# Kernel optimization log

Measured on AMD Instinct MI355X. Metric: run time of the kernel, lower is better.

The kernel has to match this reference:

```python
import jax, jax.numpy as jnp
import numpy as np

B, N, D = 4, 2048, 512
H = 8
DH = D // H
FF = 2 * D


def setup_inputs() -> dict:
    key = jax.random.key(0)
    ks = jax.random.split(key, 16)
    s = lambda fan_in: 1.0 / np.sqrt(fan_in)
    inp = {
        "x0": jax.random.normal(ks[0], (B, N, D), jnp.float32),
        "x1": jax.random.normal(ks[1], (B, N, D), jnp.float32),
        # projections (torch Linear: weight [out, in])
        "Wqk": jax.random.uniform(ks[2], (D, D), jnp.float32, -s(D), s(D)),
        "bqk": jax.random.uniform(ks[3], (D,), jnp.float32, -s(D), s(D)),
        "Wv": jax.random.uniform(ks[4], (D, D), jnp.float32, -s(D), s(D)),
        "bv": jax.random.uniform(ks[5], (D,), jnp.float32, -s(D), s(D)),
        "Wo": jax.random.uniform(ks[6], (D, D), jnp.float32, -s(D), s(D)),
        "bo": jax.random.uniform(ks[7], (D,), jnp.float32, -s(D), s(D)),
        # FFN: Linear(2D,2D) -> LayerNorm(2D) -> GELU -> Linear(2D,D)
        "Wf1": jax.random.uniform(ks[8], (FF, FF), jnp.float32, -s(FF), s(FF)),
        "bf1": jax.random.uniform(ks[9], (FF,), jnp.float32, -s(FF), s(FF)),
        "ln_g": jnp.ones((FF,), jnp.float32),
        "ln_b": jnp.zeros((FF,), jnp.float32),
        "Wf2": jax.random.uniform(ks[10], (D, FF), jnp.float32, -s(FF), s(FF)),
        "bf2": jax.random.uniform(ks[11], (D,), jnp.float32, -s(FF), s(FF)),
    }
    return inp


def _split_heads(t):
    # [B,N,D] -> [B,H,N,DH]
    return t.reshape(B, N, H, DH).transpose(0, 2, 1, 3)


def _attn(q, k, v):
    # q,k,v: [B,H,N,DH]; scale by sqrt(d_k) as in the torch Attention module
    scores = jnp.einsum("bhnd,bhmd->bhnm", q, k) / jnp.sqrt(jnp.float32(DH))
    attn = jax.nn.softmax(scores, axis=-1)
    return jnp.einsum("bhnm,bhmd->bhnd", attn, v)


def _merge_heads(t):
    # [B,H,N,DH] -> [B,N,D]
    return t.transpose(0, 2, 1, 3).reshape(B, N, D)


def _ffn(x, Wf1, bf1, ln_g, ln_b, Wf2, bf2):
    h = x @ Wf1.T + bf1
    mu = jnp.mean(h, axis=-1, keepdims=True)
    var = jnp.mean(jnp.square(h - mu), axis=-1, keepdims=True)
    h = (h - mu) / jnp.sqrt(var + 1e-5) * ln_g + ln_b
    h = jax.nn.gelu(h, approximate=False)
    return h @ Wf2.T + bf2


def reference(x0, x1, Wqk, bqk, Wv, bv, Wo, bo, Wf1, bf1, ln_g, ln_b, Wf2, bf2):
    qk0 = _split_heads(x0 @ Wqk.T + bqk)
    qk1 = _split_heads(x1 @ Wqk.T + bqk)
    v0 = _split_heads(x0 @ Wv.T + bv)
    v1 = _split_heads(x1 @ Wv.T + bv)

    m0 = _merge_heads(_attn(qk0, qk1, v1)) @ Wo.T + bo
    m1 = _merge_heads(_attn(qk1, qk0, v0)) @ Wo.T + bo

    y0 = x0 + _ffn(jnp.concatenate([x0, m0], -1), Wf1, bf1, ln_g, ln_b, Wf2, bf2)
    y1 = x1 + _ffn(jnp.concatenate([x1, m1], -1), Wf1, bf1, ln_g, ln_b, Wf2, bf2)
    return (y0, y1)
```

## Files before the change

kernel.cpp:

```cpp
#include <hip/hip_runtime.h>
#include <hip/hip_bf16.h>
#include <math.h>

typedef __bf16 bf16;
typedef __bf16 bf16x8 __attribute__((ext_vector_type(8)));
typedef __bf16 bf16x4 __attribute__((ext_vector_type(4)));
typedef float  f32x4  __attribute__((ext_vector_type(4)));

#define DEVI __device__ __forceinline__

DEVI void async16(bf16* lds, const bf16* g) {
    __builtin_amdgcn_global_load_lds(
        (const __attribute__((address_space(1))) unsigned int*)g,
        (__attribute__((address_space(3))) unsigned int*)lds, 16, 0, 0);
}
DEVI f32x4 mfma16(bf16x8 a, bf16x8 b, f32x4 c) {
    return __builtin_amdgcn_mfma_f32_16x16x32_bf16(a, b, c, 0, 0, 0);
}

__global__ __launch_bounds__(256) void prep(
    const float* __restrict__ x0, const float* __restrict__ x1, bf16* __restrict__ Xbf,
    const float* __restrict__ Wqk, const float* __restrict__ Wv,
    const float* __restrict__ Wf1, const float* __restrict__ Wf2,
    bf16* __restrict__ Wqkv, bf16* __restrict__ Wbig, bf16* __restrict__ Wf1Rb,
    bf16* __restrict__ Wf2b,
    const float* __restrict__ Wo, bf16* __restrict__ WoT,
    const float* __restrict__ bo, const float* __restrict__ bf1,
    float* __restrict__ bf1p)
{
    __shared__ float Ls[64][65];
    const int bid = blockIdx.x, t = threadIdx.x;
    if (bid < 8192) {
        long i = (long)bid * 256 + t;
        long r = i >> 7, c = (i & 127) * 4;
        const float* src = (r < 8192) ? (x0 + r * 512 + c) : (x1 + (r - 8192) * 512 + c);
        float4 v = *(const float4*)src;
        bf16x4 o;
        o[0] = (bf16)v.x; o[1] = (bf16)v.y; o[2] = (bf16)v.z; o[3] = (bf16)v.w;
        *(bf16x4*)(Xbf + r * 1024 + c) = o;
    } else if (bid < 10240) {
        long i = (long)(bid - 8192) * 256 + t;
        const float* s; bf16* d;
        if (i < 131072) {
            s = (i < 65536) ? Wqk + i * 4 : Wv + (i - 65536) * 4;
            d = Wqkv + i * 4;
        } else if (i < 393216) {
            long e = (i - 131072) * 4, r = e >> 10, c = e & 1023;
            s = Wf1 + e;
            d = (c < 512) ? (Wbig + r * 1024 + c) : (Wf1Rb + r * 512 + (c - 512));
        } else {
            s = Wf2 + (i - 393216) * 4;
            d = Wf2b + (i - 393216) * 4;
        }
        float4 v = *(const float4*)s;
        bf16x4 o;
        o[0] = (bf16)v.x; o[1] = (bf16)v.y; o[2] = (bf16)v.z; o[3] = (bf16)v.w;
        *(bf16x4*)d = o;
    } else if (bid < 10304) {
        const int bb = bid - 10240;
        const int bi = bb & 7, bj = bb >> 3;
        const int i0 = bi * 64, j0 = bj * 64;
        const int r0 = t >> 4, c4 = (t & 15) * 4;
#pragma unroll
        for (int it = 0; it < 4; it++) {
            int row = r0 + 16 * it;
            float4 v = *(const float4*)(Wo + (long)(i0 + row) * 512 + j0 + c4);
            Ls[row][c4] = v.x; Ls[row][c4 + 1] = v.y;
            Ls[row][c4 + 2] = v.z; Ls[row][c4 + 3] = v.w;
        }
        __syncthreads();
#pragma unroll
        for (int it = 0; it < 4; it++) {
            int orow = r0 + 16 * it;
            bf16x4 o;
#pragma unroll
            for (int k = 0; k < 4; k++) o[k] = (bf16)Ls[c4 + k][orow];
            *(bf16x4*)(WoT + (long)(j0 + orow) * 512 + i0 + c4) = o;
        }
    } else {
        const int w = t >> 6, lane = t & 63;
        const int row = (bid - 10304) * 4 + w;
        const float* rp = Wf1 + (long)row * 1024 + 512 + lane * 8;
        float4 a = *(const float4*)rp;
        float4 b = *(const float4*)(rp + 4);
        const float* bp = bo + lane * 8;
        float4 c = *(const float4*)bp;
        float4 d = *(const float4*)(bp + 4);
        float s = a.x * c.x + a.y * c.y + a.z * c.z + a.w * c.w +
                  b.x * d.x + b.y * d.y + b.z * d.z + b.w * d.w;
#pragma unroll
        for (int k = 1; k < 64; k <<= 1) s += __shfl_xor(s, k);
        if (lane == 0) bf1p[row] = bf1[row] + s;
    }
}

template <int MODE>
__global__ __launch_bounds__(256) void gemm_bt(
    const bf16* __restrict__ A, long lda,
    const bf16* __restrict__ B, long ldb,
    const float* __restrict__ bias,
    void* __restrict__ Cout, long ldc,
    const float* __restrict__ res0, const float* __restrict__ res1,
    const float* __restrict__ bias2, void* __restrict__ Cout2,
    int M, int N, int K, float scale)
{
    __shared__ bf16 As[128 * 64];
    __shared__ bf16 Bs[128 * 64];
    const int t = threadIdx.x;
    const int w = t >> 6, lane = t & 63, quad = lane >> 4, m15 = lane & 15;
    const int wm = w >> 1, wn = w & 1;
    const int nbx = N >> 7;
    const int xcd = blockIdx.x & 7, local = blockIdx.x >> 3;
    const int mtiles_per_xcd = (int)(gridDim.x >> 3) / nbx;
    const int by = xcd * mtiles_per_xcd + local / nbx;
    const int bx = local % nbx;
    const long m0 = (long)by * 128, n0 = (long)bx * 128;

    f32x4 acc[4][4] = {};

    for (int k0 = 0; k0 < K; k0 += 64) {
#pragma unroll
        for (int i = 0; i < 4; i++) {
            int idx = i * 256 + t, row = idx >> 3, p = idx & 7;
            int gc = k0 + ((p ^ (row & 7)) * 8);
            async16(As + idx * 8, A + (m0 + row) * lda + gc);
            async16(Bs + idx * 8, B + (n0 + row) * ldb + gc);
        }
        __syncthreads();
#pragma unroll
        for (int kk = 0; kk < 2; kk++) {
            bf16x8 af[4], bfr[4];
#pragma unroll
            for (int mt = 0; mt < 4; mt++) {
                int row = wm * 64 + mt * 16 + m15;
                af[mt] = *(const bf16x8*)(As + row * 64 + (((kk * 4 + quad) ^ (row & 7)) * 8));
            }
#pragma unroll
            for (int nt = 0; nt < 4; nt++) {
                int row = wn * 64 + nt * 16 + m15;
                bfr[nt] = *(const bf16x8*)(Bs + row * 64 + (((kk * 4 + quad) ^ (row & 7)) * 8));
            }
#pragma unroll
            for (int mt = 0; mt < 4; mt++)
#pragma unroll
                for (int nt = 0; nt < 4; nt++)
                    acc[mt][nt] = mfma16(af[mt], bfr[nt], acc[mt][nt]);
        }
        __syncthreads();
    }

#pragma unroll
    for (int nt = 0; nt < 4; nt++) {
        long col = n0 + wn * 64 + nt * 16 + m15;
#pragma unroll
        for (int mt = 0; mt < 4; mt++) {
            long row = m0 + wm * 64 + mt * 16 + quad * 4;
            if (MODE == 0) {
                bf16* C = (bf16*)Cout;
                float bs = bias[col];
#pragma unroll
                for (int r = 0; r < 4; r++)
                    C[(row + r) * ldc + col] = (bf16)(acc[mt][nt][r] + bs);
            } else if (MODE == 4) {
                bf16* C = (bf16*)Cout;
#pragma unroll
                for (int r = 0; r < 4; r++)
                    C[(row + r) * ldc + col] = (bf16)acc[mt][nt][r];
            } else if (MODE == 5) {
                if (col < 512) {
                    bf16* C = (bf16*)Cout;
                    float bs = bias[col];
#pragma unroll
                    for (int r = 0; r < 4; r++)
                        C[(row + r) * ldc + col] = (bf16)((acc[mt][nt][r] + bs) * scale);
                } else {
                    bf16* V = (bf16*)Cout2;
                    long v = col - 512;
                    float bs = bias2[v];
                    bf16x4 pv;
#pragma unroll
                    for (int r = 0; r < 4; r++) pv[r] = (bf16)(acc[mt][nt][r] + bs);
                    *(bf16x4*)(V + v * 16384 + row) = pv;
                }
            } else {
                float* C = (float*)Cout;
                float bs = bias[col];
#pragma unroll
                for (int r = 0; r < 4; r++) {
                    long grow = row + r;
                    const float* rs = (grow < 8192) ? (res0 + grow * 512)
                                                    : (res1 + (grow - 8192) * 512);
                    C[grow * ldc + col] = acc[mt][nt][r] + bs + rs[col];
                }
            }
        }
    }
}

__global__ __launch_bounds__(256, 4) void flash_attn(const bf16* __restrict__ QK,
                                                     const bf16* __restrict__ VT,
                                                     bf16* __restrict__ o)
{
    __shared__ bf16 lds[16384];
    bf16* Ks = lds;
    bf16* Vs = lds + 4096;
    bf16* Ps = lds + 8192;

    const int t = threadIdx.x, w = t >> 6, lane = t & 63;
    const int quad = lane >> 4, m15 = lane & 15;
    const int bid = blockIdx.x;
    const int qt5 = bid & 15;
    const int h   = (bid >> 4) & 7;
    const int b   = (bid >> 7) & 3;
    const int dir = bid >> 9;
    const long qrow0  = (long)dir * 8192 + b * 2048 + qt5 * 128;
    const long kvrow0 = (long)(1 - dir) * 8192 + b * 2048;
    const int hc = h * 64;

#pragma unroll
    for (int i = 0; i < 4; i++) {
        int idx = i * 256 + t, row = idx >> 3, p = idx & 7;
        async16(lds + idx * 8, QK + (qrow0 + row) * 512 + hc + ((p ^ (row & 7)) * 8));
    }
    __syncthreads();
    bf16x8 qf[2][2];
#pragma unroll
    for (int qt = 0; qt < 2; qt++)
#pragma unroll
        for (int kh = 0; kh < 2; kh++) {
            int row = w * 32 + qt * 16 + m15;
            qf[qt][kh] = *(const bf16x8*)(lds + row * 64 + (((kh * 4 + quad) ^ (row & 7)) * 8));
        }
    __syncthreads();

    f32x4 oacc[4][2] = {};
    float lrun[2] = {0.f, 0.f};

    for (int kb = 0; kb < 32; kb++) {
        const long key0 = kvrow0 + kb * 64;
#pragma unroll
        for (int i = 0; i < 2; i++) {
            int idx = i * 256 + t, row = idx >> 3, p = idx & 7;
            async16(Ks + idx * 8, QK + (key0 + row) * 512 + hc + ((p ^ (row & 7)) * 8));
        }
#pragma unroll
        for (int i = 0; i < 2; i++) {
            int idx = i * 256 + t, row = idx >> 3, p = idx & 7;
            async16(Vs + idx * 8, VT + (long)(hc + row) * 16384 + key0 + ((p ^ (row & 7)) * 8));
        }
        __syncthreads();

        f32x4 s[4][2];
#pragma unroll
        for (int mt = 0; mt < 4; mt++) {
            int row = mt * 16 + m15;
            bf16x8 kf0 = *(const bf16x8*)(Ks + row * 64 + ((quad ^ (row & 7)) * 8));
            bf16x8 kf1 = *(const bf16x8*)(Ks + row * 64 + (((4 + quad) ^ (row & 7)) * 8));
#pragma unroll
            for (int qt = 0; qt < 2; qt++) {
                f32x4 z = {0.f, 0.f, 0.f, 0.f};
                z = mfma16(kf0, qf[qt][0], z);
                s[mt][qt] = mfma16(kf1, qf[qt][1], z);
            }
        }

#pragma unroll
        for (int qt = 0; qt < 2; qt++) {
            float rs = 0.f;
#pragma unroll
            for (int mt = 0; mt < 4; mt++)
#pragma unroll
                for (int r = 0; r < 4; r++) {
                    float p = exp2f(s[mt][qt][r]);
                    s[mt][qt][r] = p;
                    rs += p;
                }
            rs += __shfl_xor(rs, 16);
            rs += __shfl_xor(rs, 32);
            lrun[qt] += rs;
        }

        bf16* Pw = Ps + w * 2048;
#pragma unroll
        for (int qt = 0; qt < 2; qt++) {
            int ql = qt * 16 + m15;
#pragma unroll
            for (int mt = 0; mt < 4; mt++) {
                bf16x4 pv;
#pragma unroll
                for (int r = 0; r < 4; r++) pv[r] = (bf16)s[mt][qt][r];
                int u = (mt * 2 + (quad >> 1)) ^ (ql & 7);
                *(bf16x4*)(Pw + ql * 64 + u * 8 + (quad & 1) * 4) = pv;
            }
        }
        asm volatile("s_waitcnt lgkmcnt(0)" ::: "memory");

#pragma unroll
        for (int kc = 0; kc < 2; kc++) {
            bf16x8 pf[2];
#pragma unroll
            for (int qt = 0; qt < 2; qt++) {
                int ql = qt * 16 + m15;
                pf[qt] = *(const bf16x8*)(Pw + ql * 64 + (((kc * 4 + quad) ^ (ql & 7)) * 8));
            }
#pragma unroll
            for (int dt = 0; dt < 4; dt++) {
                int vrow = dt * 16 + m15;
                bf16x8 vf = *(const bf16x8*)(Vs + vrow * 64 + (((kc * 4 + quad) ^ (vrow & 7)) * 8));
#pragma unroll
                for (int qt = 0; qt < 2; qt++)
                    oacc[dt][qt] = mfma16(pf[qt], vf, oacc[dt][qt]);
            }
        }
        __syncthreads();
    }

#pragma unroll
    for (int qt = 0; qt < 2; qt++)
#pragma unroll
        for (int r = 0; r < 4; r++) {
            float li = __shfl(lrun[qt], quad * 4 + r);
            float inv = 1.f / li;
            long row = qrow0 + w * 32 + qt * 16 + quad * 4 + r;
#pragma unroll
            for (int dt = 0; dt < 4; dt++)
                o[row * 1024 + hc + dt * 16 + m15] = (bf16)(oacc[dt][qt][r] * inv);
        }
}

__global__ __launch_bounds__(256) void ln_gelu(bf16* __restrict__ H,
                                               const float* __restrict__ g,
                                               const float* __restrict__ bta)
{
    const int row = blockIdx.x, t = threadIdx.x;
    const int w = t >> 6, lane = t & 63;
    bf16* hp = H + (long)row * 1024 + t * 4;
    bf16x4 hv = *(const bf16x4*)hp;
    float h[4];
#pragma unroll
    for (int j = 0; j < 4; j++) h[j] = (float)hv[j];
    float s1 = h[0] + h[1] + h[2] + h[3];
    float s2 = h[0] * h[0] + h[1] * h[1] + h[2] * h[2] + h[3] * h[3];
#pragma unroll
    for (int d = 1; d < 64; d <<= 1) {
        s1 += __shfl_xor(s1, d);
        s2 += __shfl_xor(s2, d);
    }
    __shared__ float rbuf[8];
    if (lane == 0) { rbuf[w] = s1; rbuf[4 + w] = s2; }
    __syncthreads();
    s1 = rbuf[0] + rbuf[1] + rbuf[2] + rbuf[3];
    s2 = rbuf[4] + rbuf[5] + rbuf[6] + rbuf[7];
    const float mu = s1 * (1.f / 1024.f);
    const float var = s2 * (1.f / 1024.f) - mu * mu;
    const float rstd = rsqrtf(var + 1e-5f);
    bf16x4 out;
#pragma unroll
    for (int j = 0; j < 4; j++) {
        int c = t * 4 + j;
        float x = (h[j] - mu) * rstd * g[c] + bta[c];
        float y = 0.5f * x * (1.f + erff(x * 0.70710678118654752f));
        out[j] = (bf16)y;
    }
    *(bf16x4*)hp = out;
}

extern "C" void kernel_launch(void* const* d_in, const int* in_sizes, int n_in,
                              void* d_out, int out_size, void* d_ws, size_t ws_size,
                              hipStream_t stream)
{
    const float* x0  = (const float*)d_in[0];
    const float* x1  = (const float*)d_in[1];
    const float* Wqk = (const float*)d_in[2];
    const float* bqk = (const float*)d_in[3];
    const float* Wv  = (const float*)d_in[4];
    const float* bv  = (const float*)d_in[5];
    const float* Wo  = (const float*)d_in[6];
    const float* bo  = (const float*)d_in[7];
    const float* Wf1 = (const float*)d_in[8];
    const float* bf1 = (const float*)d_in[9];
    const float* lng = (const float*)d_in[10];
    const float* lnb = (const float*)d_in[11];
    const float* Wf2 = (const float*)d_in[12];
    const float* bf2 = (const float*)d_in[13];

    char* ws = (char*)d_ws;
    bf16* Xbf   = (bf16*)ws; ws += 16384L * 1024 * 2;
    bf16* QKbf  = (bf16*)ws;
    bf16* Hbuf  = (bf16*)ws;
    ws += 16384L * 512 * 2;
    bf16* VtG   = (bf16*)ws; ws += 16384L * 512 * 2;
    bf16* Wqkv  = (bf16*)ws; ws += 1024L * 512 * 2;
    bf16* Wbig  = (bf16*)ws; ws += 1024L * 1024 * 2;
    bf16* Wf1Rb = (bf16*)ws; ws += 1024L * 512 * 2;
    bf16* Wf2b  = (bf16*)ws; ws += 512L * 1024 * 2;
    bf16* WoT   = (bf16*)ws; ws += 512L * 512 * 2;
    float* bf1p = (float*)ws; ws += 1024 * 4;

    const float qs = 0.42466090014400953f;

    prep<<<10560, 256, 0, stream>>>(x0, x1, Xbf, Wqk, Wv, Wf1, Wf2,
                                    Wqkv, Wbig, Wf1Rb, Wf2b, Wo, WoT, bo, bf1, bf1p);

    gemm_bt<4><<<32, 256, 0, stream>>>(Wf1Rb, 512, WoT, 512, nullptr,
                                       Wbig + 512, 1024, nullptr, nullptr,
                                       nullptr, nullptr, 1024, 512, 512, 1.f);

    gemm_bt<5><<<1024, 256, 0, stream>>>(Xbf, 1024, Wqkv, 512, bqk,
                                         QKbf, 512, nullptr, nullptr,
                                         bv, VtG, 16384, 1024, 512, qs);

    flash_attn<<<1024, 256, 0, stream>>>(QKbf, VtG, Xbf + 512);

    gemm_bt<0><<<1024, 256, 0, stream>>>(Xbf, 1024, Wbig, 1024, bf1p,
                                         Hbuf, 1024, nullptr, nullptr,
                                         nullptr, nullptr, 16384, 1024, 1024, 1.f);
    ln_gelu<<<16384, 256, 0, stream>>>(Hbuf, lng, lnb);
    gemm_bt<1><<<512, 256, 0, stream>>>(Hbuf, 1024, Wf2b, 1024, bf2,
                                        d_out, 512, x0, x1,
                                        nullptr, nullptr, 16384, 512, 1024, 1.f);
}
```

Baseline: 369.4 us.

## Double-buffer K tiles in flash attention and compute row sums via MFMA

Doubles the K shared-memory buffer so the next key tile is prefetched while the current one is used. The V load is overlapped with the QK^T and softmax stages, using split vmcnt waits and raw barriers instead of __syncthreads. The softmax denominator is now accumulated with an MFMA against a ones vector, which removes the per-iteration shuffle reductions, and s_setprio hints are added around the MFMA sections. The costs are more LDS per block (possibly lower occupancy) and an extra redundant K prefetch on the last iteration. The row sum also now uses the bf16-rounded probabilities, which matches what multiplies V.

```diff
diff --git a/kernel.cpp b/kernel.cpp
--- a/kernel.cpp
+++ b/kernel.cpp
@@ -201,10 +201,10 @@
                                                      const bf16* __restrict__ VT,
                                                      bf16* __restrict__ o)
 {
-    __shared__ bf16 lds[16384];
+    __shared__ bf16 lds[20480];
     bf16* Ks = lds;
-    bf16* Vs = lds + 4096;
-    bf16* Ps = lds + 8192;
+    bf16* Vs = lds + 8192;
+    bf16* Ps = lds + 12288;
 
     const int t = threadIdx.x, w = t >> 6, lane = t & 63;
     const int quad = lane >> 4, m15 = lane & 15;
@@ -233,29 +233,46 @@
         }
     __syncthreads();
 
+#pragma unroll
+    for (int i = 0; i < 2; i++) {
+        int idx = i * 256 + t, row = idx >> 3, p = idx & 7;
+        async16(Ks + idx * 8, QK + (kvrow0 + row) * 512 + hc + ((p ^ (row & 7)) * 8));
+    }
+
     f32x4 oacc[4][2] = {};
-    float lrun[2] = {0.f, 0.f};
-
+    f32x4 racc[2] = {};
+    bf16x8 ones;
+#pragma unroll
+    for (int j = 0; j < 8; j++) ones[j] = (bf16)1.0f;
+
+    int cur = 0;
     for (int kb = 0; kb < 32; kb++) {
-        const long key0 = kvrow0 + kb * 64;
-#pragma unroll
-        for (int i = 0; i < 2; i++) {
-            int idx = i * 256 + t, row = idx >> 3, p = idx & 7;
-            async16(Ks + idx * 8, QK + (key0 + row) * 512 + hc + ((p ^ (row & 7)) * 8));
-        }
+        const long key0  = kvrow0 + kb * 64;
+        const long key0n = kvrow0 + ((kb + 1) & 31) * 64;
+        bf16* Kc = Ks + cur * 4096;
+        bf16* Kn = Ks + (cur ^ 1) * 4096;
+
+        asm volatile("s_waitcnt vmcnt(0)" ::: "memory");
+        __builtin_amdgcn_s_barrier();
+
 #pragma unroll
         for (int i = 0; i < 2; i++) {
             int idx = i * 256 + t, row = idx >> 3, p = idx & 7;
             async16(Vs + idx * 8, VT + (long)(hc + row) * 16384 + key0 + ((p ^ (row & 7)) * 8));
         }
-        __syncthreads();
+#pragma unroll
+        for (int i = 0; i < 2; i++) {
+            int idx = i * 256 + t, row = idx >> 3, p = idx & 7;
+            async16(Kn + idx * 8, QK + (key0n + row) * 512 + hc + ((p ^ (row & 7)) * 8));
+        }
 
         f32x4 s[4][2];
+        __builtin_amdgcn_s_setprio(1);
 #pragma unroll
         for (int mt = 0; mt < 4; mt++) {
             int row = mt * 16 + m15;
-            bf16x8 kf0 = *(const bf16x8*)(Ks + row * 64 + ((quad ^ (row & 7)) * 8));
-            bf16x8 kf1 = *(const bf16x8*)(Ks + row * 64 + (((4 + quad) ^ (row & 7)) * 8));
+            bf16x8 kf0 = *(const bf16x8*)(Kc + row * 64 + ((quad ^ (row & 7)) * 8));
+            bf16x8 kf1 = *(const bf16x8*)(Kc + row * 64 + (((4 + quad) ^ (row & 7)) * 8));
 #pragma unroll
             for (int qt = 0; qt < 2; qt++) {
                 f32x4 z = {0.f, 0.f, 0.f, 0.f};
@@ -263,22 +280,15 @@
                 s[mt][qt] = mfma16(kf1, qf[qt][1], z);
             }
         }
-
-#pragma unroll
-        for (int qt = 0; qt < 2; qt++) {
-            float rs = 0.f;
+        __builtin_amdgcn_s_setprio(0);
+
+#pragma unroll
+        for (int qt = 0; qt < 2; qt++)
 #pragma unroll
             for (int mt = 0; mt < 4; mt++)
 #pragma unroll
-                for (int r = 0; r < 4; r++) {
-                    float p = exp2f(s[mt][qt][r]);
-                    s[mt][qt][r] = p;
-                    rs += p;
-                }
-            rs += __shfl_xor(rs, 16);
-            rs += __shfl_xor(rs, 32);
-            lrun[qt] += rs;
-        }
+                for (int r = 0; r < 4; r++)
+                    s[mt][qt][r] = exp2f(s[mt][qt][r]);
 
         bf16* Pw = Ps + w * 2048;
 #pragma unroll
@@ -293,8 +303,10 @@
                 *(bf16x4*)(Pw + ql * 64 + u * 8 + (quad & 1) * 4) = pv;
             }
         }
-        asm volatile("s_waitcnt lgkmcnt(0)" ::: "memory");
-
+        asm volatile("s_waitcnt vmcnt(2) lgkmcnt(0)" ::: "memory");
+        __builtin_amdgcn_s_barrier();
+
+        __builtin_amdgcn_s_setprio(1);
 #pragma unroll
         for (int kc = 0; kc < 2; kc++) {
             bf16x8 pf[2];
@@ -304,6 +316,9 @@
                 pf[qt] = *(const bf16x8*)(Pw + ql * 64 + (((kc * 4 + quad) ^ (ql & 7)) * 8));
             }
 #pragma unroll
+            for (int qt = 0; qt < 2; qt++)
+                racc[qt] = mfma16(pf[qt], ones, racc[qt]);
+#pragma unroll
             for (int dt = 0; dt < 4; dt++) {
                 int vrow = dt * 16 + m15;
                 bf16x8 vf = *(const bf16x8*)(Vs + vrow * 64 + (((kc * 4 + quad) ^ (vrow & 7)) * 8));
@@ -312,15 +327,15 @@
                     oacc[dt][qt] = mfma16(pf[qt], vf, oacc[dt][qt]);
             }
         }
-        __syncthreads();
+        __builtin_amdgcn_s_setprio(0);
+        cur ^= 1;
     }
 
 #pragma unroll
     for (int qt = 0; qt < 2; qt++)
 #pragma unroll
         for (int r = 0; r < 4; r++) {
-            float li = __shfl(lrun[qt], quad * 4 + r);
-            float inv = 1.f / li;
+            float inv = 1.f / racc[qt][r];
             long row = qrow0 + w * 32 + qt * 16 + quad * 4 + r;
 #pragma unroll
             for (int dt = 0; dt < 4; dt++)
```

Result: no change. 367.8 us (-0.4%).
